# Optimization experiments

Measured on AMD Instinct MI355X. Metric: run time of the kernel, lower is better.

## Reference

```python
import jax, jax.numpy as jnp
import numpy as np

KERNEL_MUL = 2.0
KERNEL_NUM = 5


def setup_inputs() -> dict:
    key = jax.random.key(0)
    k1, k2 = jax.random.split(key)
    source = jax.random.normal(k1, (4096, 256), dtype=jnp.float32)
    target = jax.random.normal(k2, (4096, 256), dtype=jnp.float32)
    return {"source": source, "target": target}


def _mmd(source, target):
    b = source.shape[0]
    total = jnp.concatenate([source, target], axis=0)  # [2N, D]
    n = total.shape[0]
    # pairwise squared L2 via gram trick (avoids O(N^2 * D) intermediate)
    sq = jnp.sum(total * total, axis=1)  # [2N]
    d2 = sq[:, None] + sq[None, :] - 2.0 * (total @ total.T)
    d2 = jnp.maximum(d2, 0.0)  # [2N, 2N]
    # bandwidth from detached distances (matches L2_distance.data)
    bandwidth = jax.lax.stop_gradient(jnp.sum(d2)) / (n * n - n)
    bandwidth = bandwidth / (KERNEL_MUL ** (KERNEL_NUM // 2))
    kernels = jnp.zeros_like(d2)
    for i in range(KERNEL_NUM):
        kernels = kernels + jnp.exp(-d2 / (bandwidth * KERNEL_MUL ** i))
    XX = kernels[:b, :b]
    YY = kernels[b:, b:]
    XY = kernels[:b, b:]
    YX = kernels[b:, :b]
    return jnp.mean(XX + YY - XY - YX)


def reference(source, target):
    return _mmd(source, target)
```

## Files before the change

kernel.cpp:

```cpp
#include <hip/hip_runtime.h>
#include <hip/hip_bf16.h>


#define N_TOTAL 8192
#define B_HALF 4096
#define D_DIM 256
#define TILE 128
#define NTILE 64
#define NTRI 2080

typedef float f32x16 __attribute__((ext_vector_type(16)));
typedef _Float16 f16x8 __attribute__((ext_vector_type(8)));

__device__ __forceinline__ const float* row_base(const float* src, const float* tgt, int r) {
    return (r < B_HALF) ? src + (size_t)r * D_DIM : tgt + (size_t)(r - B_HALF) * D_DIM;
}

__global__ __launch_bounds__(256) void prep_kernel(const float* __restrict__ src,
                                                   const float* __restrict__ tgt,
                                                   _Float16* __restrict__ a16f,
                                                   float* __restrict__ sq,
                                                   float* __restrict__ colpart) {
    __shared__ float cpl[4][D_DIM];
    int tid = threadIdx.x, w = tid >> 6, lane = tid & 63;
    int r0 = blockIdx.x * 32;

    float c0 = 0.f, c1 = 0.f, c2 = 0.f, c3 = 0.f;
    #pragma unroll
    for (int i = 0; i < 8; ++i) {
        int row = r0 + w * 8 + i;
        const float* rp = row_base(src, tgt, row);
        float4 v = ((const float4*)rp)[lane];
        c0 += v.x; c1 += v.y; c2 += v.z; c3 += v.w;
        float s = v.x*v.x + v.y*v.y + v.z*v.z + v.w*v.w;
        #pragma unroll
        for (int off = 32; off; off >>= 1) s += __shfl_down(s, off, 64);
        if (lane == 0) sq[row] = s;
    }
    cpl[w][lane * 4 + 0] = c0;
    cpl[w][lane * 4 + 1] = c1;
    cpl[w][lane * 4 + 2] = c2;
    cpl[w][lane * 4 + 3] = c3;
    __syncthreads();
    colpart[blockIdx.x * D_DIM + tid] =
        cpl[0][tid] + cpl[1][tid] + cpl[2][tid] + cpl[3][tid];

    int wg = blockIdx.x * 4 + w;
    #pragma unroll
    for (int i = 0; i < 4; ++i) {
        int t  = wg * 4 + i;
        int kb = t >> 7, rg = t & 127;
        int row = rg * 64 + lane;
        const float* rp = row_base(src, tgt, row) + kb * 8;
        float4 v0 = ((const float4*)rp)[0];
        float4 v1 = ((const float4*)rp)[1];
        _Float16 h[8] = {(_Float16)v0.x, (_Float16)v0.y, (_Float16)v0.z, (_Float16)v0.w,
                         (_Float16)v1.x, (_Float16)v1.y, (_Float16)v1.z, (_Float16)v1.w};
        *(f16x8*)(a16f + ((size_t)kb * N_TOTAL + row) * 8) = *(f16x8*)h;
    }
}

__global__ __launch_bounds__(256) void bw_kernel(const float* __restrict__ sq,
                                                 const float* __restrict__ colpart,
                                                 float* __restrict__ negc,
                                                 double* __restrict__ accum) {
    __shared__ double red[256];
    int t = threadIdx.x;
    double s = 0.0;
    for (int i = t; i < N_TOTAL; i += 256) s += (double)sq[i];
    red[t] = s;
    __syncthreads();
    for (int off = 128; off; off >>= 1) {
        if (t < off) red[t] += red[t + off];
        __syncthreads();
    }
    double sumsq = red[0];
    __syncthreads();
    float c = 0.f;
    for (int k = 0; k < 256; ++k) c += colpart[k * D_DIM + t];
    red[t] = (double)c * (double)c;
    __syncthreads();
    for (int off = 128; off; off >>= 1) {
        if (t < off) red[t] += red[t + off];
        __syncthreads();
    }
    if (t == 0) {
        double S1 = 2.0 * (double)N_TOTAL * sumsq - 2.0 * red[0];
        double nn = (double)N_TOTAL * (double)N_TOTAL - (double)N_TOTAL;
        double bw = S1 / nn / 4.0;
        negc[0] = (float)(-1.4426950408889634 / (16.0 * bw));
        accum[0] = 0.0;
    }
}

__global__ __launch_bounds__(256, 4) void mmd_main(const _Float16* __restrict__ a16f,
                                                   const float* __restrict__ sq,
                                                   const float* __restrict__ negc,
                                                   double* __restrict__ accum) {
    __shared__ float wsum[4];

    int b  = blockIdx.x;
    int bs = (b & 7) * (NTRI / 8) + (b >> 3);
    int it = 0, cum = 0;
    while (cum + (NTILE - it) <= bs) { cum += NTILE - it; ++it; }
    int jt = it + (bs - cum);

    int tid = threadIdx.x, lane = tid & 63, wid = tid >> 6;
    int wrow = wid >> 1, wcol = wid & 1;
    int rowA = it * TILE, rowB = jt * TILE;
    int c32 = lane & 31, khalf = lane >> 5;

    const _Float16* PA = a16f + (size_t)khalf * (N_TOTAL * 8)
                              + (size_t)(rowA + wrow * 64 + c32) * 8;
    const _Float16* PB = a16f + (size_t)khalf * (N_TOTAL * 8)
                              + (size_t)(rowB + wcol * 64 + c32) * 8;

    f32x16 acc[2][2] = {};

    #pragma unroll 4
    for (int kap = 0; kap < 16; ++kap) {
        size_t ko = (size_t)kap * (N_TOTAL * 16);
        f16x8 af[2], bf[2];
        af[0] = *(const f16x8*)(PA + ko);
        af[1] = *(const f16x8*)(PA + ko + 32 * 8);
        bf[0] = *(const f16x8*)(PB + ko);
        bf[1] = *(const f16x8*)(PB + ko + 32 * 8);
        __builtin_amdgcn_s_setprio(1);
        #pragma unroll
        for (int mt = 0; mt < 2; ++mt)
            #pragma unroll
            for (int nt = 0; nt < 2; ++nt)
                acc[mt][nt] = __builtin_amdgcn_mfma_f32_32x32x16_f16(af[mt], bf[nt], acc[mt][nt], 0, 0, 0);
        __builtin_amdgcn_s_setprio(0);
    }

    float nc = *negc;
    float m2nc = -2.f * nc;
    float sj1[2];
    #pragma unroll
    for (int nt = 0; nt < 2; ++nt)
        sj1[nt] = nc * sq[rowB + wcol * 64 + nt * 32 + c32];
    float tu = 0.f, t2 = 0.f;
    #pragma unroll
    for (int mt = 0; mt < 2; ++mt) {
        #pragma unroll
        for (int reg = 0; reg < 16; ++reg) {
            int i = rowA + wrow * 64 + mt * 32 + (reg & 3) + 8 * (reg >> 2) + 4 * khalf;
            float si1 = nc * sq[i];
            #pragma unroll
            for (int nt = 0; nt < 2; ++nt) {
                float e  = fminf(fmaf(m2nc, acc[mt][nt][reg], si1 + sj1[nt]), 0.f);
                float u  = exp2f(e);
                float u2 = u * u, u4 = u2 * u2, u8 = u4 * u4;
                float in2 = fmaf(u4, 1.f + u8, 1.f);
                float in3 = fmaf(u2, in2, 1.f);
                tu += u;
                t2  = fmaf(u2, in3, t2);
            }
        }
    }
    float scale = (((it < 32) == (jt < 32)) ? 1.f : -1.f) * ((it == jt) ? 1.f : 2.f);
    float tsum = (tu + t2) * scale;

    #pragma unroll
    for (int off = 32; off; off >>= 1) tsum += __shfl_down(tsum, off, 64);
    if (lane == 0) wsum[wid] = tsum;
    __syncthreads();
    if (tid == 0) {
        float t = wsum[0] + wsum[1] + wsum[2] + wsum[3];
        atomicAdd(accum, (double)t);
    }
}

__global__ void finalize_kernel(const double* __restrict__ accum, float* __restrict__ out) {
    out[0] = (float)(accum[0] / ((double)B_HALF * (double)B_HALF));
}

extern "C" void kernel_launch(void* const* d_in, const int* in_sizes, int n_in,
                              void* d_out, int out_size, void* d_ws, size_t ws_size,
                              hipStream_t stream) {
    const float* src = (const float*)d_in[0];
    const float* tgt = (const float*)d_in[1];
    float* out = (float*)d_out;

    char* ws = (char*)d_ws;
    float*    sq      = (float*)ws;
    float*    colpart = (float*)(ws + 32768);
    float*    negc    = (float*)(ws + 294912);
    double*   accum   = (double*)(ws + 294920);
    _Float16* a16f    = (_Float16*)(ws + 327680);

    prep_kernel<<<256, 256, 0, stream>>>(src, tgt, a16f, sq, colpart);
    bw_kernel<<<1, 256, 0, stream>>>(sq, colpart, negc, accum);
    mmd_main<<<NTRI, 256, 0, stream>>>(a16f, sq, negc, accum);
    finalize_kernel<<<1, 1, 0, stream>>>(accum, out);
}
```

Before: 71.93 us.

## Fold bandwidth and finalize kernels into prep and main via last-block atomics

Removes the separate bandwidth-reduction and finalize kernel launches. Prep blocks now atomically accumulate the sum of squares and column sums, and the last block to finish computes the bandwidth constant. The main kernel uses a completion counter so its last block writes the output. A memset is added to zero the metadata, and float atomics make the column-sum reduction order nondeterministic.

After: 98.14 us. 36.4% more time.

```diff
diff --git a/kernel.cpp b/kernel.cpp
--- a/kernel.cpp
+++ b/kernel.cpp
@@ -12,6 +12,7 @@
 typedef float f32x16 __attribute__((ext_vector_type(16)));
 typedef _Float16 f16x8 __attribute__((ext_vector_type(8)));
 
+
 __device__ __forceinline__ const float* row_base(const float* src, const float* tgt, int r) {
     return (r < B_HALF) ? src + (size_t)r * D_DIM : tgt + (size_t)(r - B_HALF) * D_DIM;
 }
@@ -20,12 +21,20 @@
                                                    const float* __restrict__ tgt,
                                                    _Float16* __restrict__ a16f,
                                                    float* __restrict__ sq,
-                                                   float* __restrict__ colpart) {
+                                                   char* __restrict__ meta) {
+    double*   accum  = (double*)meta;           (void)accum;
+    double*   sumsq  = (double*)(meta + 8);
+    unsigned* cntp   = (unsigned*)(meta + 16);
+    float*    colsum = (float*)(meta + 64);
+    float*    negc   = (float*)(meta + 1152);
+
     __shared__ float cpl[4][D_DIM];
+    __shared__ int islast;
     int tid = threadIdx.x, w = tid >> 6, lane = tid & 63;
     int r0 = blockIdx.x * 32;
 
     float c0 = 0.f, c1 = 0.f, c2 = 0.f, c3 = 0.f;
+    float sq_part = 0.f;
     #pragma unroll
     for (int i = 0; i < 8; ++i) {
         int row = r0 + w * 8 + i;
@@ -35,15 +44,39 @@
         float s = v.x*v.x + v.y*v.y + v.z*v.z + v.w*v.w;
         #pragma unroll
         for (int off = 32; off; off >>= 1) s += __shfl_down(s, off, 64);
-        if (lane == 0) sq[row] = s;
+        if (lane == 0) { sq[row] = s; sq_part += s; }
     }
     cpl[w][lane * 4 + 0] = c0;
     cpl[w][lane * 4 + 1] = c1;
     cpl[w][lane * 4 + 2] = c2;
     cpl[w][lane * 4 + 3] = c3;
-    __syncthreads();
-    colpart[blockIdx.x * D_DIM + tid] =
-        cpl[0][tid] + cpl[1][tid] + cpl[2][tid] + cpl[3][tid];
+    if (lane == 0) atomicAdd(sumsq, (double)sq_part);
+    __syncthreads();
+    atomicAdd(&colsum[tid], cpl[0][tid] + cpl[1][tid] + cpl[2][tid] + cpl[3][tid]);
+
+    __syncthreads();
+    if (tid == 0) {
+        unsigned old = atomicAdd(cntp, 1u);
+        islast = (old == 255u);
+    }
+    __syncthreads();
+    if (islast) {
+        __shared__ float red[256];
+        float c = atomicAdd(&colsum[tid], 0.f);
+        red[tid] = c * c;
+        __syncthreads();
+        for (int off = 128; off; off >>= 1) {
+            if (tid < off) red[tid] += red[tid + off];
+            __syncthreads();
+        }
+        if (tid == 0) {
+            double ss = atomicAdd(sumsq, 0.0);
+            double S1 = 2.0 * (double)N_TOTAL * ss - 2.0 * (double)red[0];
+            double nn = (double)N_TOTAL * (double)N_TOTAL - (double)N_TOTAL;
+            double bw = S1 / nn / 4.0;
+            negc[0] = (float)(-1.4426950408889634 / (16.0 * bw));
+        }
+    }
 
     int wg = blockIdx.x * 4 + w;
     #pragma unroll
@@ -60,43 +93,14 @@
     }
 }
 
-__global__ __launch_bounds__(256) void bw_kernel(const float* __restrict__ sq,
-                                                 const float* __restrict__ colpart,
-                                                 float* __restrict__ negc,
-                                                 double* __restrict__ accum) {
-    __shared__ double red[256];
-    int t = threadIdx.x;
-    double s = 0.0;
-    for (int i = t; i < N_TOTAL; i += 256) s += (double)sq[i];
-    red[t] = s;
-    __syncthreads();
-    for (int off = 128; off; off >>= 1) {
-        if (t < off) red[t] += red[t + off];
-        __syncthreads();
-    }
-    double sumsq = red[0];
-    __syncthreads();
-    float c = 0.f;
-    for (int k = 0; k < 256; ++k) c += colpart[k * D_DIM + t];
-    red[t] = (double)c * (double)c;
-    __syncthreads();
-    for (int off = 128; off; off >>= 1) {
-        if (t < off) red[t] += red[t + off];
-        __syncthreads();
-    }
-    if (t == 0) {
-        double S1 = 2.0 * (double)N_TOTAL * sumsq - 2.0 * red[0];
-        double nn = (double)N_TOTAL * (double)N_TOTAL - (double)N_TOTAL;
-        double bw = S1 / nn / 4.0;
-        negc[0] = (float)(-1.4426950408889634 / (16.0 * bw));
-        accum[0] = 0.0;
-    }
-}
-
 __global__ __launch_bounds__(256, 4) void mmd_main(const _Float16* __restrict__ a16f,
                                                    const float* __restrict__ sq,
-                                                   const float* __restrict__ negc,
-                                                   double* __restrict__ accum) {
+                                                   char* __restrict__ meta,
+                                                   float* __restrict__ out) {
+    double*   accum = (double*)meta;
+    unsigned* cntm  = (unsigned*)(meta + 20);
+    const float* negc = (const float*)(meta + 1152);
+
     __shared__ float wsum[4];
 
     int b  = blockIdx.x;
@@ -169,11 +173,13 @@
     if (tid == 0) {
         float t = wsum[0] + wsum[1] + wsum[2] + wsum[3];
         atomicAdd(accum, (double)t);
-    }
-}
-
-__global__ void finalize_kernel(const double* __restrict__ accum, float* __restrict__ out) {
-    out[0] = (float)(accum[0] / ((double)B_HALF * (double)B_HALF));
+        asm volatile("s_waitcnt vmcnt(0)" ::: "memory");
+        unsigned old = atomicAdd(cntm, 1u);
+        if (old == NTRI - 1) {
+            double v = atomicAdd(accum, 0.0);
+            out[0] = (float)(v / ((double)B_HALF * (double)B_HALF));
+        }
+    }
 }
 
 extern "C" void kernel_launch(void* const* d_in, const int* in_sizes, int n_in,
@@ -184,14 +190,11 @@
     float* out = (float*)d_out;
 
     char* ws = (char*)d_ws;
-    float*    sq      = (float*)ws;
-    float*    colpart = (float*)(ws + 32768);
-    float*    negc    = (float*)(ws + 294912);
-    double*   accum   = (double*)(ws + 294920);
-    _Float16* a16f    = (_Float16*)(ws + 327680);
-
-    prep_kernel<<<256, 256, 0, stream>>>(src, tgt, a16f, sq, colpart);
-    bw_kernel<<<1, 256, 0, stream>>>(sq, colpart, negc, accum);
-    mmd_main<<<NTRI, 256, 0, stream>>>(a16f, sq, negc, accum);
-    finalize_kernel<<<1, 1, 0, stream>>>(accum, out);
-}
+    char*     meta = ws;
+    float*    sq   = (float*)(ws + 4096);
+    _Float16* a16f = (_Float16*)(ws + 65536);
+
+    hipMemsetAsync(meta, 0, 1088, stream);
+    prep_kernel<<<256, 256, 0, stream>>>(src, tgt, a16f, sq, meta);
+    mmd_main<<<NTRI, 256, 0, stream>>>(a16f, sq, meta, out);
+}
```
